# Kernel optimization log

Measured on AMD Instinct MI355X. Metric: run time of the kernel, lower is better.

Reference implementation:

```python
import jax, jax.numpy as jnp
import numpy as np

H = 64  # LSTM hidden size (hardcoded in Baseline)

def _lstm_encode(x, W_ih, W_hh, b_ih, b_hh):
    # x: [N, C, T] -> final hidden state [N, H]
    # PyTorch LSTMCell gate order: i, f, g, o
    N = x.shape[0]
    xs = jnp.moveaxis(x, 2, 0)                       # [T, N, C]
    xp = jnp.einsum('tnc,gc->tng', xs, W_ih) + b_ih  # precompute input proj [T, N, 4H]
    h0 = jnp.zeros((N, H), dtype=x.dtype)
    c0 = jnp.zeros((N, H), dtype=x.dtype)

    def step(carry, xp_t):
        h, c = carry
        g = xp_t + h @ W_hh.T + b_hh                 # [N, 4H]
        i, f, gg, o = jnp.split(g, 4, axis=-1)
        c = jax.nn.sigmoid(f) * c + jax.nn.sigmoid(i) * jnp.tanh(gg)
        h = jax.nn.sigmoid(o) * jnp.tanh(c)
        return (h, c), None

    (h, _), _ = jax.lax.scan(step, (h0, c0), xp)
    return h

def _head(x, W1, b1, W2, b2, W3, b3):
    # dropout is identity at inference; relu on first two layers, none on last
    x = jax.nn.relu(x @ W1.T + b1)
    x = jax.nn.relu(x @ W2.T + b2)
    return x @ W3.T + b3

def setup_inputs() -> dict:
    key = jax.random.key(0)
    ks = jax.random.split(key, 24)
    C1, C2 = 32, 56
    N, T = 8192, 72
    d = {
        'X_obs': jax.random.normal(ks[0], (N, C1, T), jnp.float32),
        'X_wrf_cmaq': jax.random.normal(ks[1], (N, C2, T), jnp.float32),
        'obs_Wih': jax.random.normal(ks[2], (4 * H, C1), jnp.float32) * 0.1,
        'obs_Whh': jax.random.normal(ks[3], (4 * H, H), jnp.float32) * 0.1,
        'obs_bih': jax.random.normal(ks[4], (4 * H,), jnp.float32) * 0.1,
        'obs_bhh': jax.random.normal(ks[5], (4 * H,), jnp.float32) * 0.1,
        'wrf_Wih': jax.random.normal(ks[6], (4 * H, C2), jnp.float32) * 0.1,
        'wrf_Whh': jax.random.normal(ks[7], (4 * H, H), jnp.float32) * 0.1,
        'wrf_bih': jax.random.normal(ks[8], (4 * H,), jnp.float32) * 0.1,
        'wrf_bhh': jax.random.normal(ks[9], (4 * H,), jnp.float32) * 0.1,
    }
    dims = [(96, 128), (64, 96), (48, 64)]
    k = 10
    for head in ('fsp', 'o3'):
        for li, (o, i) in enumerate(dims, 1):
            d[f'{head}_W{li}'] = jax.random.normal(ks[k], (o, i), jnp.float32) * (1.0 / np.sqrt(i)); k += 1
            d[f'{head}_b{li}'] = jax.random.normal(ks[k], (o,), jnp.float32) * 0.05; k += 1
    return d

def reference(X_obs, X_wrf_cmaq,
              obs_Wih, obs_Whh, obs_bih, obs_bhh,
              wrf_Wih, wrf_Whh, wrf_bih, wrf_bhh,
              fsp_W1, fsp_b1, fsp_W2, fsp_b2, fsp_W3, fsp_b3,
              o3_W1, o3_b1, o3_W2, o3_b2, o3_W3, o3_b3):
    h_obs = _lstm_encode(X_obs, obs_Wih, obs_Whh, obs_bih, obs_bhh)
    h_wrf = _lstm_encode(X_wrf_cmaq, wrf_Wih, wrf_Whh, wrf_bih, wrf_bhh)
    feat = jnp.concatenate([h_obs, h_wrf], axis=1)  # [N, 128]
    fsp = _head(feat, fsp_W1, fsp_b1, fsp_W2, fsp_b2, fsp_W3, fsp_b3)
    o3 = _head(feat, o3_W1, o3_b1, o3_W2, o3_b2, o3_W3, o3_b3)
    return jnp.stack([fsp, o3], axis=1)  # [N, 2, 48]
```

## Files before the change

### kernel.cpp

```cpp
#include <hip/hip_runtime.h>

typedef __attribute__((ext_vector_type(8))) short short8;
typedef __attribute__((ext_vector_type(4))) float f32x4;

#define OFF_BXO   64
#define OFF_BHO   (OFF_BXO + 16384)
#define OFF_BXW   (OFF_BHO + 32768)
#define OFF_BHW   (OFF_BXW + 32768)
#define OFF_HW    (OFF_BHW + 32768)
#define OFF_BIASL (OFF_HW + 43008)
#define OFF_BIASH (OFF_BIASL + 1024)
#define OFF_FEAT  (OFF_BIASH + 832)

__device__ __forceinline__ float b2f(unsigned short u) {
    return __uint_as_float(((unsigned)u) << 16);
}
__device__ __forceinline__ unsigned short f2b(float f) {
    unsigned u = __float_as_uint(f);
    u += 0x7FFFu + ((u >> 16) & 1u);
    return (unsigned short)(u >> 16);
}
__device__ __forceinline__ float ldin(const void* p, int idx, int isf) {
    return isf ? ((const float*)p)[idx] : b2f(((const unsigned short*)p)[idx]);
}
__device__ __forceinline__ float sigmoidf_(float x) {
    return __builtin_amdgcn_rcpf(1.0f + __expf(-x));
}
__device__ __forceinline__ float tanhf_(float x) {
    return 2.0f * __builtin_amdgcn_rcpf(1.0f + __expf(-2.0f * x)) - 1.0f;
}
__device__ __forceinline__ f32x4 MFMA(short8 a, short8 b, f32x4 c) {
    return __builtin_amdgcn_mfma_f32_16x16x32_bf16(a, b, c, 0, 0, 0);
}

__global__ __launch_bounds__(256) void detect_kernel(
    const unsigned short* __restrict__ X, int* __restrict__ flag)
{
    __shared__ int cnt[256];
    int c = 0;
    for (int i = threadIdx.x; i < 2048; i += 256) {
        unsigned short u = X[2 * i];
        c += (((u >> 7) & 0xFF) >= 192);
    }
    cnt[threadIdx.x] = c;
    __syncthreads();
    if (threadIdx.x == 0) {
        int s = 0;
        for (int i = 0; i < 256; ++i) s += cnt[i];
        *flag = (s > 64) ? 1 : 0;
    }
}

__global__ __launch_bounds__(256) void prep_kernel(
    const void* oWih, const void* oWhh, const void* obih, const void* obhh,
    const void* wWih, const void* wWhh, const void* wbih, const void* wbhh,
    const void* fW1, const void* fb1, const void* fW2, const void* fb2,
    const void* fW3, const void* fb3,
    const void* oW1, const void* ob1, const void* oW2, const void* ob2,
    const void* oW3, const void* ob3,
    unsigned short* __restrict__ ws)
{
    const int isf = ((const int*)ws)[0];
    const int gid = blockIdx.x * 256 + threadIdx.x;
    const int gsz = gridDim.x * 256;

    unsigned short* BXO = ws + OFF_BXO;
    unsigned short* BHO = ws + OFF_BHO;
    unsigned short* BXW = ws + OFF_BXW;
    unsigned short* BHW = ws + OFF_BHW;
    unsigned short* HW  = ws + OFF_HW;

    for (int i = gid; i < 8192; i += gsz) {
        int j = i & 7, lane = (i >> 3) & 63, nt = (i >> 9) & 3, wave = i >> 11;
        int g = wave * 64 + nt * 16 + (lane & 15);
        int k = ((lane >> 4) << 3) + j;
        float w = ldin(oWih, g * 32 + k, isf);
        unsigned short hi = f2b(w);
        BXO[i] = hi; BXO[8192 + i] = f2b(w - b2f(hi));
    }
    for (int i = gid; i < 16384; i += gsz) {
        int j = i & 7, lane = (i >> 3) & 63, nt = (i >> 9) & 3;
        int kt = (i >> 11) & 1, wave = i >> 12;
        int g = wave * 64 + nt * 16 + (lane & 15);
        int k = kt * 32 + ((lane >> 4) << 3) + j;
        float w = ldin(oWhh, g * 64 + k, isf);
        unsigned short hi = f2b(w);
        BHO[i] = hi; BHO[16384 + i] = f2b(w - b2f(hi));
    }
    for (int i = gid; i < 16384; i += gsz) {
        int j = i & 7, lane = (i >> 3) & 63, nt = (i >> 9) & 3;
        int wave = (i >> 11) & 3, kt2 = i >> 13;
        int g = wave * 64 + nt * 16 + (lane & 15);
        int k = kt2 * 32 + ((lane >> 4) << 3) + j;
        float w = (k < 56) ? ldin(wWih, g * 56 + k, isf) : 0.f;
        unsigned short hi = f2b(w);
        BXW[i] = hi; BXW[16384 + i] = f2b(w - b2f(hi));
    }
    for (int i = gid; i < 16384; i += gsz) {
        int j = i & 7, lane = (i >> 3) & 63, nt = (i >> 9) & 3;
        int kt = (i >> 11) & 1, wave = i >> 12;
        int g = wave * 64 + nt * 16 + (lane & 15);
        int k = kt * 32 + ((lane >> 4) << 3) + j;
        float w = ldin(wWhh, g * 64 + k, isf);
        unsigned short hi = f2b(w);
        BHW[i] = hi; BHW[16384 + i] = f2b(w - b2f(hi));
    }
    for (int i = gid; i < 12288; i += gsz) HW[i]         = f2b(ldin(fW1, i, isf));
    for (int i = gid; i < 6144;  i += gsz) HW[12288 + i] = f2b(ldin(fW2, i, isf));
    for (int i = gid; i < 3072;  i += gsz) HW[18432 + i] = f2b(ldin(fW3, i, isf));
    for (int i = gid; i < 12288; i += gsz) HW[21504 + i] = f2b(ldin(oW1, i, isf));
    for (int i = gid; i < 6144;  i += gsz) HW[33792 + i] = f2b(ldin(oW2, i, isf));
    for (int i = gid; i < 3072;  i += gsz) HW[39936 + i] = f2b(ldin(oW3, i, isf));
    float* BL = (float*)(ws + OFF_BIASL);
    for (int i = gid; i < 256; i += gsz) BL[i]       = ldin(obih, i, isf) + ldin(obhh, i, isf);
    for (int i = gid; i < 256; i += gsz) BL[256 + i] = ldin(wbih, i, isf) + ldin(wbhh, i, isf);
    float* BB = (float*)(ws + OFF_BIASH);
    for (int i = gid; i < 96; i += gsz) BB[i]       = ldin(fb1, i, isf);
    for (int i = gid; i < 64; i += gsz) BB[96 + i]  = ldin(fb2, i, isf);
    for (int i = gid; i < 48; i += gsz) BB[160 + i] = ldin(fb3, i, isf);
    for (int i = gid; i < 96; i += gsz) BB[208 + i] = ldin(ob1, i, isf);
    for (int i = gid; i < 64; i += gsz) BB[304 + i] = ldin(ob2, i, isf);
    for (int i = gid; i < 48; i += gsz) BB[368 + i] = ldin(ob3, i, isf);
}

#define TCH 4
__global__ __launch_bounds__(256) void lstm_kernel(
    const void* __restrict__ Xo, const void* __restrict__ Xw,
    unsigned short* __restrict__ ws)
{
    __shared__ unsigned short xbuf[2][TCH][8][16][8];
    __shared__ float gates[256][16];
    __shared__ unsigned short hfrag[2][2][4][16][8];

    const int tid  = threadIdx.x;
    const int wave = tid >> 6, lane = tid & 63;
    const int quad = lane >> 4, m16 = lane & 15;
    const bool isw = blockIdx.x >= 512;
    const int blk  = isw ? (int)blockIdx.x - 512 : (int)blockIdx.x;
    const int n0   = blk * 16;
    const int isf  = ((const int*)ws)[0];

    const void* x = isw ? Xw : Xo;
    const unsigned short* BX = ws + (isw ? OFF_BXW : OFF_BXO);
    const unsigned short* BH = ws + (isw ? OFF_BHW : OFF_BHO);
    const float* BL = (const float*)(ws + OFF_BIASL) + (isw ? 256 : 0);
    unsigned short* featH = ws + OFF_FEAT;
    unsigned short* featL = featH + 8192 * 128;
    const int C       = isw ? 56 : 32;
    const int Cpad    = isw ? 64 : 32;
    const int cshift  = isw ? 6 : 5;
    const int xloOff  = isw ? 16384 : 8192;
    const int featOff = isw ? 64 : 0;

    short8 BhH[2][4], BhL[2][4];
#pragma unroll
    for (int kt = 0; kt < 2; ++kt)
#pragma unroll
        for (int nt = 0; nt < 4; ++nt) {
            int idx = ((wave * 2 + kt) * 4 + nt) * 512 + lane * 8;
            BhH[kt][nt] = *(const short8*)&BH[idx];
            BhL[kt][nt] = *(const short8*)&BH[16384 + idx];
        }
    short8 BxH0[4], BxL0[4], BxH1[4], BxL1[4];
#pragma unroll
    for (int nt = 0; nt < 4; ++nt) {
        int idx = (wave * 4 + nt) * 512 + lane * 8;
        BxH0[nt] = *(const short8*)&BX[idx];
        BxL0[nt] = *(const short8*)&BX[xloOff + idx];
    }
    if (isw) {
#pragma unroll
        for (int nt = 0; nt < 4; ++nt) {
            int idx = (wave * 4 + nt) * 512 + lane * 8;
            BxH1[nt] = *(const short8*)&BX[8192 + idx];
            BxL1[nt] = *(const short8*)&BX[xloOff + 8192 + idx];
        }
    }

    const int j0  = tid >> 2;
    const int nlo = (tid & 3) * 4;
    const float bias_i = BL[j0];
    const float bias_f = BL[j0 + 64];
    const float bias_g = BL[j0 + 128];
    const float bias_o = BL[j0 + 192];
    float c4[4] = {0.f, 0.f, 0.f, 0.f};

    const int colr = (tid & 3) ^ ((j0 >> 1) & 3);
    const int hchunkbit = ((j0 >> 3) & 1) << 2;
    const int prr = ((((m16 & 3) << 2) | (m16 >> 2)) ^ ((quad & 1) << 2));

    for (int i = tid; i < 2 * 2 * 4 * 16 * 8; i += 256)
        ((unsigned short*)hfrag)[i] = 0;

    for (int chunk = 0; chunk < 18; ++chunk) {
        const int t0 = chunk * TCH;
        for (int i = tid; i < (16 << cshift); i += 256) {
            int n = i >> cshift, c = i & (Cpad - 1);
            float v[TCH];
            if (c < C) {
                size_t off = ((size_t)(n0 + n) * C + c) * 72 + t0;
                if (isf) {
                    f32x4 u0 = *(const f32x4*)((const float*)x + off);
                    v[0] = u0[0]; v[1] = u0[1]; v[2] = u0[2]; v[3] = u0[3];
                } else {
                    const unsigned short* p = (const unsigned short*)x + off;
#pragma unroll
                    for (int j = 0; j < TCH; ++j) v[j] = b2f(p[j]);
                }
            } else {
#pragma unroll
                for (int j = 0; j < TCH; ++j) v[j] = 0.f;
            }
            int kt = c >> 3;
            int pr = n ^ kt;
#pragma unroll
            for (int tt = 0; tt < TCH; ++tt) {
                unsigned short hi = f2b(v[tt]);
                xbuf[0][tt][kt][pr][c & 7] = hi;
                xbuf[1][tt][kt][pr][c & 7] = f2b(v[tt] - b2f(hi));
            }
        }
        __syncthreads();

        for (int tt = 0; tt < TCH; ++tt) {
            const int t = t0 + tt;
            f32x4 acc[4] = {{0,0,0,0},{0,0,0,0},{0,0,0,0},{0,0,0,0}};
            {
                short8 axh = *(const short8*)&xbuf[0][tt][quad][m16 ^ quad][0];
                short8 axl = *(const short8*)&xbuf[1][tt][quad][m16 ^ quad][0];
#pragma unroll
                for (int nt = 0; nt < 4; ++nt) {
                    acc[nt] = MFMA(axh, BxH0[nt], acc[nt]);
                    acc[nt] = MFMA(axl, BxH0[nt], acc[nt]);
                    acc[nt] = MFMA(axh, BxL0[nt], acc[nt]);
                }
            }
            if (isw) {
                short8 axh = *(const short8*)&xbuf[0][tt][4 + quad][m16 ^ (4 + quad)][0];
                short8 axl = *(const short8*)&xbuf[1][tt][4 + quad][m16 ^ (4 + quad)][0];
#pragma unroll
                for (int nt = 0; nt < 4; ++nt) {
                    acc[nt] = MFMA(axh, BxH1[nt], acc[nt]);
                    acc[nt] = MFMA(axl, BxH1[nt], acc[nt]);
                    acc[nt] = MFMA(axh, BxL1[nt], acc[nt]);
                }
            }
#pragma unroll
            for (int kt = 0; kt < 2; ++kt) {
                short8 ahi = *(const short8*)&hfrag[0][kt][quad][prr][0];
                short8 alo = *(const short8*)&hfrag[1][kt][quad][prr][0];
#pragma unroll
                for (int nt = 0; nt < 4; ++nt) {
                    acc[nt] = MFMA(ahi, BhH[kt][nt], acc[nt]);
                    acc[nt] = MFMA(alo, BhH[kt][nt], acc[nt]);
                    acc[nt] = MFMA(ahi, BhL[kt][nt], acc[nt]);
                }
            }
            {
                int colw = quad ^ ((m16 >> 1) & 3);
#pragma unroll
                for (int nt = 0; nt < 4; ++nt) {
                    int g = wave * 64 + nt * 16 + m16;
                    *(f32x4*)&gates[g][colw * 4] = acc[nt];
                }
            }
            __syncthreads();

            f32x4 gi = *(f32x4*)&gates[j0][colr * 4];
            f32x4 gf = *(f32x4*)&gates[j0 + 64][colr * 4];
            f32x4 gg = *(f32x4*)&gates[j0 + 128][colr * 4];
            f32x4 go = *(f32x4*)&gates[j0 + 192][colr * 4];
#pragma unroll
            for (int e = 0; e < 4; ++e) {
                float iv = sigmoidf_(gi[e] + bias_i);
                float fv = sigmoidf_(gf[e] + bias_f);
                float gv = tanhf_(gg[e] + bias_g);
                float ov = sigmoidf_(go[e] + bias_o);
                float c  = fv * c4[e] + iv * gv;
                c4[e]    = c;
                float h  = ov * tanhf_(c);
                unsigned short hi = f2b(h);
                unsigned short lo = f2b(h - b2f(hi));
                int m = nlo + e;
                int pr = (((m & 3) << 2) | (m >> 2)) ^ hchunkbit;
                hfrag[0][j0 >> 5][(j0 >> 3) & 3][pr][j0 & 7] = hi;
                hfrag[1][j0 >> 5][(j0 >> 3) & 3][pr][j0 & 7] = lo;
                if (t == 71) {
                    featH[(size_t)(n0 + m) * 128 + featOff + j0] = hi;
                    featL[(size_t)(n0 + m) * 128 + featOff + j0] = lo;
                }
            }
            __syncthreads();
        }
    }
}

__global__ __launch_bounds__(256) void heads_kernel(
    const unsigned short* __restrict__ ws, void* __restrict__ out)
{
    __shared__ unsigned short afrag[4][4][4][16][8];
    const int tid  = threadIdx.x;
    const int wave = tid >> 6, lane = tid & 63;
    const int quad = lane >> 4, m16 = lane & 15;
    const int r0   = blockIdx.x * 64 + wave * 16;
    const int isf  = ((const int*)ws)[0];

    const unsigned short* HW    = ws + OFF_HW;
    const float*          BB    = (const float*)(ws + OFF_BIASH);
    const unsigned short* featH = ws + OFF_FEAT;
    const unsigned short* featL = featH + 8192 * 128;

    short8 fh[4], fl[4];
#pragma unroll
    for (int kt = 0; kt < 4; ++kt) {
        size_t o = (size_t)(r0 + m16) * 128 + kt * 32 + quad * 8;
        fh[kt] = *(const short8*)&featH[o];
        fl[kt] = *(const short8*)&featL[o];
    }

    for (int head = 0; head < 2; ++head) {
        const unsigned short* W1 = HW + (head ? 21504 : 0);
        const unsigned short* W2 = W1 + 12288;
        const unsigned short* W3 = W2 + 6144;
        const float* b1 = BB + head * 208;
        const float* b2 = b1 + 96;
        const float* b3 = b2 + 64;

        f32x4 a1[6] = {{0,0,0,0},{0,0,0,0},{0,0,0,0},{0,0,0,0},{0,0,0,0},{0,0,0,0}};
#pragma unroll
        for (int kt = 0; kt < 4; ++kt)
#pragma unroll
            for (int nt = 0; nt < 6; ++nt) {
                short8 bw = *(const short8*)
                    &W1[(nt * 16 + m16) * 128 + kt * 32 + quad * 8];
                a1[nt] = MFMA(fh[kt], bw, a1[nt]);
                a1[nt] = MFMA(fl[kt], bw, a1[nt]);
            }
#pragma unroll
        for (int nt = 0; nt < 6; ++nt) {
            int u = nt * 16 + m16;
            float bv = b1[u];
#pragma unroll
            for (int r = 0; r < 4; ++r) {
                float v = a1[nt][r] + bv;
                v = v > 0.f ? v : 0.f;
                afrag[wave][u >> 5][(u >> 3) & 3][quad * 4 + r][u & 7] = f2b(v);
            }
        }
        __syncthreads();

        f32x4 a2[4] = {{0,0,0,0},{0,0,0,0},{0,0,0,0},{0,0,0,0}};
#pragma unroll
        for (int kt = 0; kt < 3; ++kt) {
            short8 a = *(const short8*)&afrag[wave][kt][quad][m16][0];
#pragma unroll
            for (int nt = 0; nt < 4; ++nt) {
                short8 bw = *(const short8*)
                    &W2[(nt * 16 + m16) * 96 + kt * 32 + quad * 8];
                a2[nt] = MFMA(a, bw, a2[nt]);
            }
        }
        __syncthreads();
#pragma unroll
        for (int nt = 0; nt < 4; ++nt) {
            int u = nt * 16 + m16;
            float bv = b2[u];
#pragma unroll
            for (int r = 0; r < 4; ++r) {
                float v = a2[nt][r] + bv;
                v = v > 0.f ? v : 0.f;
                afrag[wave][u >> 5][(u >> 3) & 3][quad * 4 + r][u & 7] = f2b(v);
            }
        }
        __syncthreads();

        f32x4 a3[3] = {{0,0,0,0},{0,0,0,0},{0,0,0,0}};
#pragma unroll
        for (int kt = 0; kt < 2; ++kt) {
            short8 a = *(const short8*)&afrag[wave][kt][quad][m16][0];
#pragma unroll
            for (int nt = 0; nt < 3; ++nt) {
                short8 bw = *(const short8*)
                    &W3[(nt * 16 + m16) * 64 + kt * 32 + quad * 8];
                a3[nt] = MFMA(a, bw, a3[nt]);
            }
        }
#pragma unroll
        for (int nt = 0; nt < 3; ++nt) {
            int u = nt * 16 + m16;
            float bv = b3[u];
#pragma unroll
            for (int r = 0; r < 4; ++r) {
                int row = quad * 4 + r;
                size_t idx = (size_t)(r0 + row) * 96 + head * 48 + u;
                float v = a3[nt][r] + bv;
                if (isf) ((float*)out)[idx] = v;
                else     ((unsigned short*)out)[idx] = f2b(v);
            }
        }
        __syncthreads();
    }
}

extern "C" void kernel_launch(void* const* d_in, const int* in_sizes, int n_in,
                              void* d_out, int out_size, void* d_ws, size_t ws_size,
                              hipStream_t stream)
{
    unsigned short* ws = (unsigned short*)d_ws;

    detect_kernel<<<1, 256, 0, stream>>>((const unsigned short*)d_in[0], (int*)d_ws);
    prep_kernel<<<64, 256, 0, stream>>>(
        d_in[2], d_in[3], d_in[4], d_in[5],
        d_in[6], d_in[7], d_in[8], d_in[9],
        d_in[10], d_in[11], d_in[12], d_in[13], d_in[14], d_in[15],
        d_in[16], d_in[17], d_in[18], d_in[19], d_in[20], d_in[21],
        ws);
    lstm_kernel<<<1024, 256, 0, stream>>>(d_in[0], d_in[1], ws);
    heads_kernel<<<128, 256, 0, stream>>>(ws, d_out);
}
```

Measured before the change: 532.1 us.

## Permute LSTM gate columns so each wave computes its gates in registers

Reorders the packed recurrent and input weight fragments so each wave's four MFMA output tiles hold the i, f, g and o gates for the same hidden units. Each wave can then apply the cell update directly from its accumulators, with no gates shared-memory round trip. The hidden-state fragment buffer is double-buffered by parity, which removes one of the two barriers per timestep. The bf16 hi part is now produced by truncation rather than round-to-nearest, and the lo part carries the residual, so precision should stay close to before.

```diff
diff --git a/kernel.cpp b/kernel.cpp
--- a/kernel.cpp
+++ b/kernel.cpp
@@ -72,7 +72,7 @@
 
     for (int i = gid; i < 8192; i += gsz) {
         int j = i & 7, lane = (i >> 3) & 63, nt = (i >> 9) & 3, wave = i >> 11;
-        int g = wave * 64 + nt * 16 + (lane & 15);
+        int g = nt * 64 + wave * 16 + (lane & 15);
         int k = ((lane >> 4) << 3) + j;
         float w = ldin(oWih, g * 32 + k, isf);
         unsigned short hi = f2b(w);
@@ -81,7 +81,7 @@
     for (int i = gid; i < 16384; i += gsz) {
         int j = i & 7, lane = (i >> 3) & 63, nt = (i >> 9) & 3;
         int kt = (i >> 11) & 1, wave = i >> 12;
-        int g = wave * 64 + nt * 16 + (lane & 15);
+        int g = nt * 64 + wave * 16 + (lane & 15);
         int k = kt * 32 + ((lane >> 4) << 3) + j;
         float w = ldin(oWhh, g * 64 + k, isf);
         unsigned short hi = f2b(w);
@@ -90,7 +90,7 @@
     for (int i = gid; i < 16384; i += gsz) {
         int j = i & 7, lane = (i >> 3) & 63, nt = (i >> 9) & 3;
         int wave = (i >> 11) & 3, kt2 = i >> 13;
-        int g = wave * 64 + nt * 16 + (lane & 15);
+        int g = nt * 64 + wave * 16 + (lane & 15);
         int k = kt2 * 32 + ((lane >> 4) << 3) + j;
         float w = (k < 56) ? ldin(wWih, g * 56 + k, isf) : 0.f;
         unsigned short hi = f2b(w);
@@ -99,7 +99,7 @@
     for (int i = gid; i < 16384; i += gsz) {
         int j = i & 7, lane = (i >> 3) & 63, nt = (i >> 9) & 3;
         int kt = (i >> 11) & 1, wave = i >> 12;
-        int g = wave * 64 + nt * 16 + (lane & 15);
+        int g = nt * 64 + wave * 16 + (lane & 15);
         int k = kt * 32 + ((lane >> 4) << 3) + j;
         float w = ldin(wWhh, g * 64 + k, isf);
         unsigned short hi = f2b(w);
@@ -129,8 +129,7 @@
     unsigned short* __restrict__ ws)
 {
     __shared__ unsigned short xbuf[2][TCH][8][16][8];
-    __shared__ float gates[256][16];
-    __shared__ unsigned short hfrag[2][2][4][16][8];
+    __shared__ unsigned short hfrag[2][2][2][4][16][8];
 
     const int tid  = threadIdx.x;
     const int wave = tid >> 6, lane = tid & 63;
@@ -177,21 +176,23 @@
         }
     }
 
-    const int j0  = tid >> 2;
-    const int nlo = (tid & 3) * 4;
-    const float bias_i = BL[j0];
-    const float bias_f = BL[j0 + 64];
-    const float bias_g = BL[j0 + 128];
-    const float bias_o = BL[j0 + 192];
+    const int u = wave * 16 + m16;
+    const float bias_i = BL[u];
+    const float bias_f = BL[u + 64];
+    const float bias_g = BL[u + 128];
+    const float bias_o = BL[u + 192];
     float c4[4] = {0.f, 0.f, 0.f, 0.f};
 
-    const int colr = (tid & 3) ^ ((j0 >> 1) & 3);
-    const int hchunkbit = ((j0 >> 3) & 1) << 2;
+    const int ktw = wave >> 1;
+    const int qaw = ((wave & 1) << 1) | (m16 >> 3);
+    const int jw  = m16 & 7;
+    const int chunkbit = (m16 >> 3) << 2;
     const int prr = ((((m16 & 3) << 2) | (m16 >> 2)) ^ ((quad & 1) << 2));
 
-    for (int i = tid; i < 2 * 2 * 4 * 16 * 8; i += 256)
+    for (int i = tid; i < 2 * 2 * 2 * 4 * 16 * 8; i += 256)
         ((unsigned short*)hfrag)[i] = 0;
 
+    int par = 0;
     for (int chunk = 0; chunk < 18; ++chunk) {
         const int t0 = chunk * TCH;
         for (int i = tid; i < (16 << cshift); i += 256) {
@@ -247,8 +248,8 @@
             }
 #pragma unroll
             for (int kt = 0; kt < 2; ++kt) {
-                short8 ahi = *(const short8*)&hfrag[0][kt][quad][prr][0];
-                short8 alo = *(const short8*)&hfrag[1][kt][quad][prr][0];
+                short8 ahi = *(const short8*)&hfrag[par][0][kt][quad][prr][0];
+                short8 alo = *(const short8*)&hfrag[par][1][kt][quad][prr][0];
 #pragma unroll
                 for (int nt = 0; nt < 4; ++nt) {
                     acc[nt] = MFMA(ahi, BhH[kt][nt], acc[nt]);
@@ -256,41 +257,31 @@
                     acc[nt] = MFMA(ahi, BhL[kt][nt], acc[nt]);
                 }
             }
-            {
-                int colw = quad ^ ((m16 >> 1) & 3);
-#pragma unroll
-                for (int nt = 0; nt < 4; ++nt) {
-                    int g = wave * 64 + nt * 16 + m16;
-                    *(f32x4*)&gates[g][colw * 4] = acc[nt];
+
+#pragma unroll
+            for (int r = 0; r < 4; ++r) {
+                float iv = sigmoidf_(acc[0][r] + bias_i);
+                float fv = sigmoidf_(acc[1][r] + bias_f);
+                float gv = tanhf_(acc[2][r] + bias_g);
+                float ov = sigmoidf_(acc[3][r] + bias_o);
+                float c  = fv * c4[r] + iv * gv;
+                c4[r]    = c;
+                float h  = ov * tanhf_(c);
+                unsigned hu = __float_as_uint(h);
+                unsigned short hi = (unsigned short)(hu >> 16);
+                float hiv = __uint_as_float(hu & 0xFFFF0000u);
+                unsigned short lo = (unsigned short)(__float_as_uint(h - hiv) >> 16);
+                int pr = ((r << 2) | quad) ^ chunkbit;
+                hfrag[par ^ 1][0][ktw][qaw][pr][jw] = hi;
+                hfrag[par ^ 1][1][ktw][qaw][pr][jw] = lo;
+                if (t == 71) {
+                    int m = quad * 4 + r;
+                    featH[(size_t)(n0 + m) * 128 + featOff + u] = hi;
+                    featL[(size_t)(n0 + m) * 128 + featOff + u] = lo;
                 }
             }
             __syncthreads();
-
-            f32x4 gi = *(f32x4*)&gates[j0][colr * 4];
-            f32x4 gf = *(f32x4*)&gates[j0 + 64][colr * 4];
-            f32x4 gg = *(f32x4*)&gates[j0 + 128][colr * 4];
-            f32x4 go = *(f32x4*)&gates[j0 + 192][colr * 4];
-#pragma unroll
-            for (int e = 0; e < 4; ++e) {
-                float iv = sigmoidf_(gi[e] + bias_i);
-                float fv = sigmoidf_(gf[e] + bias_f);
-                float gv = tanhf_(gg[e] + bias_g);
-                float ov = sigmoidf_(go[e] + bias_o);
-                float c  = fv * c4[e] + iv * gv;
-                c4[e]    = c;
-                float h  = ov * tanhf_(c);
-                unsigned short hi = f2b(h);
-                unsigned short lo = f2b(h - b2f(hi));
-                int m = nlo + e;
-                int pr = (((m & 3) << 2) | (m >> 2)) ^ hchunkbit;
-                hfrag[0][j0 >> 5][(j0 >> 3) & 3][pr][j0 & 7] = hi;
-                hfrag[1][j0 >> 5][(j0 >> 3) & 3][pr][j0 & 7] = lo;
-                if (t == 71) {
-                    featH[(size_t)(n0 + m) * 128 + featOff + j0] = hi;
-                    featL[(size_t)(n0 + m) * 128 + featOff + j0] = lo;
-                }
-            }
-            __syncthreads();
+            par ^= 1;
         }
     }
 }
```

Measured after the change: 510.8 us. -4.0%, faster.
